# Optimization experiments

Hardware: AMD Instinct MI355X
Metric: run time of the kernel (lower is better)

The kernel has to match this reference:

```python
import jax, jax.numpy as jnp
import numpy as np

EPS = 1e-12

def l2norm(x, axis):
    # torch.nn.functional.normalize: x / max(||x||_2, eps)
    n = jnp.sqrt(jnp.sum(x * x, axis=axis, keepdims=True))
    return x / jnp.maximum(n, EPS)

def setup_inputs() -> dict:
    key = jax.random.key(0)
    k1, k2, k3, k4 = jax.random.split(key, 4)
    B, Cf, H, W = 128, 1024, 16, 16
    n_att, dv = 312, 300
    img = jax.random.normal(k1, (B, Cf, H, W), dtype=jnp.float32)
    # V is initialized from row-normalized w2v embeddings in the module
    V = l2norm(jax.random.normal(k2, (n_att, dv), dtype=jnp.float32), axis=1)
    W1 = jax.random.normal(k3, (dv, Cf), dtype=jnp.float32)
    W2 = jax.random.normal(k4, (dv, Cf), dtype=jnp.float32)
    return {"img": img, "V": V, "W1": W1, "W2": W2}

def reference(img, V, W1, W2):
    vv = l2norm(V, axis=1)                               # [i, v]
    B, Cf, H, Wd = img.shape
    av = l2norm(img.reshape(B, Cf, H * Wd), axis=1)      # [b, f, r]
    Q = vv @ W1                                          # [i, f]
    A = jnp.einsum('if,bfr->bir', Q, av)                 # attention logits
    A = jax.nn.softmax(A, axis=-1)
    F_p = jnp.einsum('bir,bfr->bif', A, av)              # attended features
    Pred_att = jnp.einsum('if,bif->bi', vv @ W2, F_p)
    return Pred_att
```

## Files before the change

kernel.cpp:

```cpp
#include <hip/hip_runtime.h>
#include <math.h>

#define NB   128
#define CF   1024
#define RR   256
#define NA   312
#define DV   300
#define M2   320
#define MT   640
#define NKC  32

typedef _Float16 half8  __attribute__((ext_vector_type(8)));
typedef float float16v  __attribute__((ext_vector_type(16)));

__device__ __forceinline__ void gload16(const void* g, void* l) {
    __builtin_amdgcn_global_load_lds(
        (const __attribute__((address_space(1))) void*)g,
        (__attribute__((address_space(3))) void*)l, 16, 0, 0);
}

__global__ void k_prep(const float* __restrict__ img, float* __restrict__ invg,
                       _Float16* __restrict__ avT) {
    int rc = blockIdx.x, b = blockIdx.y;
    int r0 = rc * 64;
    int t = threadIdx.x;
    __shared__ __align__(16) char sm[64 * 65 * 4];
    _Float16 (*tile)[65] = (_Float16 (*)[65])sm;
    float    (*ssb)[65]  = (float    (*)[65])sm;
    int fl = t >> 2, cg = t & 3;
    int rl = t >> 2, g  = t & 3;
    float ss[16];
    #pragma unroll
    for (int j = 0; j < 16; ++j) ss[j] = 0.f;

    for (int cc = 0; cc < 16; ++cc) {
        int f0 = cc * 64;
        const float4* p4 = (const float4*)(img + ((size_t)(b * CF + f0 + fl)) * RR + r0 + cg * 16);
        float4 v0 = p4[0], v1 = p4[1], v2 = p4[2], v3 = p4[3];
        __syncthreads();
        float xs[16] = {v0.x, v0.y, v0.z, v0.w, v1.x, v1.y, v1.z, v1.w,
                        v2.x, v2.y, v2.z, v2.w, v3.x, v3.y, v3.z, v3.w};
        #pragma unroll
        for (int j = 0; j < 16; ++j) {
            ss[j] += xs[j] * xs[j];
            tile[fl][cg * 16 + j] = (_Float16)xs[j];
        }
        __syncthreads();
        int kc  = (f0 >> 5) + (g >> 1);
        int kkb = (g & 1) * 16;
        half8 o0, o1;
        #pragma unroll
        for (int j = 0; j < 8; ++j) o0[j] = tile[g * 16 + j][rl];
        #pragma unroll
        for (int j = 0; j < 8; ++j) o1[j] = tile[g * 16 + 8 + j][rl];
        _Float16* q = avT + (((size_t)(b * NKC + kc) * RR + r0 + rl) * 32 + kkb);
        *(half8*)q       = o0;
        *(half8*)(q + 8) = o1;
    }
    __syncthreads();
    #pragma unroll
    for (int j = 0; j < 16; ++j) ssb[fl][cg * 16 + j] = ss[j];
    __syncthreads();
    if (t < 64) {
        float tot = 0.f;
        for (int f2 = 0; f2 < 64; ++f2) tot += ssb[f2][t];
        invg[b * RR + r0 + t] = 1.f / fmaxf(sqrtf(tot), 1e-12f);
    }
}

__global__ void k_q(const float* __restrict__ V, const float* __restrict__ W1,
                    const float* __restrict__ W2, _Float16* __restrict__ Qb) {
    int ib = blockIdx.x;
    int f  = blockIdx.y * 256 + threadIdx.x;
    int i0 = ib * 8;
    int t  = threadIdx.x;
    __shared__ float inv8[8];
    float acc[8] = {0,0,0,0,0,0,0,0};
    bool zero = (ib == 39 || ib == 79);
    int v0 = (ib < 40) ? i0 : i0 - M2;
    if (!zero) {
        int row = t >> 5, l32 = t & 31;
        float s = 0.f;
        for (int v = l32; v < DV; v += 32) { float x = V[(v0 + row) * DV + v]; s += x * x; }
        #pragma unroll
        for (int o = 16; o; o >>= 1) s += __shfl_xor(s, o, 32);
        if (l32 == 0) inv8[row] = 1.f / fmaxf(sqrtf(s), 1e-12f);
        __syncthreads();
        const float* W = (ib < 40) ? W1 : W2;
        for (int v = 0; v < DV; ++v) {
            float wv = W[(size_t)v * CF + f];
            #pragma unroll
            for (int ii = 0; ii < 8; ++ii) acc[ii] += V[(v0 + ii) * DV + v] * wv;
        }
        #pragma unroll
        for (int ii = 0; ii < 8; ++ii) acc[ii] *= inv8[ii];
    }
    #pragma unroll
    for (int ii = 0; ii < 8; ++ii)
        Qb[((size_t)(f >> 5) * MT + (i0 + ii)) * 32 + (f & 31)] = (_Float16)acc[ii];
}

__launch_bounds__(256, 2)
__global__ void k_gemm(const _Float16* __restrict__ Qb, const _Float16* __restrict__ avT,
                       const float* __restrict__ invg, float* __restrict__ out) {
    int lin  = blockIdx.x;
    int xcd  = lin & 7;
    int slot = lin >> 3;
    int bq   = slot / 5;
    int t2   = slot - bq * 5;
    int b    = bq * 8 + xcd;

    int tid = threadIdx.x;
    int lane = tid & 63, w = tid >> 6;
    int nl = lane & 31, kh = lane >> 5;

    __shared__ __align__(16) char smem[49152];
    _Float16* A0 = (_Float16*)smem;
    _Float16* A1 = (_Float16*)(smem + 8192);
    _Float16* B0 = (_Float16*)(smem + 16384);
    _Float16* B1 = (_Float16*)(smem + 32768);
    float* mred = (float*)smem;
    float* mg   = (float*)(smem + 1024);
    float* sred = (float*)(smem + 1280);
    float* dred = (float*)(smem + 2304);

    float16v acc[4][2];
    #pragma unroll
    for (int i = 0; i < 4; ++i)
        #pragma unroll
        for (int j = 0; j < 2; ++j)
            #pragma unroll
            for (int gi = 0; gi < 16; ++gi) acc[i][j][gi] = 0.f;

    int arow  = tid & 127;
    int akb0  = tid >> 7;
    int grow  = (arow < 64) ? (t2 * 64 + arow) : (M2 + t2 * 64 + (arow - 64));
    size_t a_src0 = (size_t)grow * 32 + akb0 * 8;
    size_t a_dst0 = ((size_t)akb0 * 128 + arow) * 8;
    size_t b_src0 = (size_t)tid * 32;
    size_t b_dst0 = (size_t)tid * 8;
    const _Float16* bpanel = avT + (size_t)b * NKC * RR * 32;

    #define STAGE(kc_, Ad, Bd) do {                                             \
        const _Float16* as = Qb + (size_t)(kc_) * MT * 32;                      \
        gload16(as + a_src0,      (Ad) + a_dst0);                               \
        gload16(as + a_src0 + 16, (Ad) + a_dst0 + 2048);                        \
        const _Float16* bs = bpanel + (size_t)(kc_) * RR * 32;                  \
        gload16(bs + b_src0 + 0 * 8, (Bd) + b_dst0 + 0 * 2048);                 \
        gload16(bs + b_src0 + 1 * 8, (Bd) + b_dst0 + 1 * 2048);                 \
        gload16(bs + b_src0 + 2 * 8, (Bd) + b_dst0 + 2 * 2048);                 \
        gload16(bs + b_src0 + 3 * 8, (Bd) + b_dst0 + 3 * 2048);                 \
    } while (0)

    #define COMPUTE(Al, Bl) do {                                                \
        _Pragma("unroll")                                                       \
        for (int ks = 0; ks < 2; ++ks) {                                        \
            int kb = ks * 2 + kh;                                               \
            half8 b0f = *(const half8*)((Bl) + ((size_t)kb * 256 + w * 64 + nl) * 8);       \
            half8 b1f = *(const half8*)((Bl) + ((size_t)kb * 256 + w * 64 + 32 + nl) * 8);  \
            _Pragma("unroll")                                                   \
            for (int rf = 0; rf < 4; ++rf) {                                    \
                half8 af = *(const half8*)((Al) + ((size_t)kb * 128 + rf * 32 + nl) * 8);   \
                acc[rf][0] = __builtin_amdgcn_mfma_f32_32x32x16_f16(af, b0f, acc[rf][0], 0, 0, 0); \
                acc[rf][1] = __builtin_amdgcn_mfma_f32_32x32x16_f16(af, b1f, acc[rf][1], 0, 0, 0); \
            }                                                                   \
        }                                                                       \
    } while (0)

    STAGE(0, A0, B0);
    for (int kc = 0; kc < NKC; kc += 2) {
        __syncthreads();
        STAGE(kc + 1, A1, B1);
        COMPUTE(A0, B0);
        __syncthreads();
        if (kc + 2 < NKC) STAGE(kc + 2, A0, B0);
        COMPUTE(A1, B1);
    }
    __syncthreads();
    #undef STAGE
    #undef COMPUTE

    float iv0 = invg[b * RR + w * 64 + nl];
    float iv1 = invg[b * RR + w * 64 + 32 + nl];
    #pragma unroll
    for (int rf = 0; rf < 4; ++rf)
        #pragma unroll
        for (int gi = 0; gi < 16; ++gi) {
            acc[rf][0][gi] *= iv0;
            acc[rf][1][gi] *= iv1;
        }

    float mx[2][16];
    #pragma unroll
    for (int p = 0; p < 2; ++p)
        #pragma unroll
        for (int gi = 0; gi < 16; ++gi)
            mx[p][gi] = fmaxf(acc[p][0][gi], acc[p][1][gi]);
    #pragma unroll
    for (int off = 1; off <= 16; off <<= 1)
        #pragma unroll
        for (int p = 0; p < 2; ++p)
            #pragma unroll
            for (int gi = 0; gi < 16; ++gi)
                mx[p][gi] = fmaxf(mx[p][gi], __shfl_xor(mx[p][gi], off, 64));
    if (nl == 0) {
        #pragma unroll
        for (int p = 0; p < 2; ++p)
            #pragma unroll
            for (int gi = 0; gi < 16; ++gi) {
                int row = (gi & 3) + 8 * (gi >> 2) + 4 * kh;
                mred[(p * 32 + row) * 4 + w] = mx[p][gi];
            }
    }
    __syncthreads();
    if (tid < 64)
        mg[tid] = fmaxf(fmaxf(mred[tid * 4], mred[tid * 4 + 1]),
                        fmaxf(mred[tid * 4 + 2], mred[tid * 4 + 3]));
    __syncthreads();
    float sp[2][16], dp[2][16];
    #pragma unroll
    for (int p = 0; p < 2; ++p)
        #pragma unroll
        for (int gi = 0; gi < 16; ++gi) {
            int row = (gi & 3) + 8 * (gi >> 2) + 4 * kh;
            float m  = mg[p * 32 + row];
            float e0 = __expf(acc[p][0][gi] - m);
            float e1 = __expf(acc[p][1][gi] - m);
            sp[p][gi] = e0 + e1;
            dp[p][gi] = e0 * acc[p + 2][0][gi] + e1 * acc[p + 2][1][gi];
        }
    #pragma unroll
    for (int off = 1; off <= 16; off <<= 1)
        #pragma unroll
        for (int p = 0; p < 2; ++p)
            #pragma unroll
            for (int gi = 0; gi < 16; ++gi) {
                sp[p][gi] += __shfl_xor(sp[p][gi], off, 64);
                dp[p][gi] += __shfl_xor(dp[p][gi], off, 64);
            }
    if (nl == 0) {
        #pragma unroll
        for (int p = 0; p < 2; ++p)
            #pragma unroll
            for (int gi = 0; gi < 16; ++gi) {
                int row = (gi & 3) + 8 * (gi >> 2) + 4 * kh;
                sred[(p * 32 + row) * 4 + w] = sp[p][gi];
                dred[(p * 32 + row) * 4 + w] = dp[p][gi];
            }
    }
    __syncthreads();
    if (tid < 64) {
        float s = sred[tid * 4] + sred[tid * 4 + 1] + sred[tid * 4 + 2] + sred[tid * 4 + 3];
        float d = dred[tid * 4] + dred[tid * 4 + 1] + dred[tid * 4 + 2] + dred[tid * 4 + 3];
        int ig = t2 * 64 + tid;
        if (ig < NA) out[b * NA + ig] = d / s;
    }
}

extern "C" void kernel_launch(void* const* d_in, const int* in_sizes, int n_in,
                              void* d_out, int out_size, void* d_ws, size_t ws_size,
                              hipStream_t stream) {
    const float* img = (const float*)d_in[0];
    const float* V   = (const float*)d_in[1];
    const float* W1  = (const float*)d_in[2];
    const float* W2  = (const float*)d_in[3];
    float* out = (float*)d_out;

    char* ws = (char*)d_ws;
    size_t off = 0;
    float*    invg = (float*)(ws + off);    off += (size_t)NB * RR * 4;
    _Float16* avT  = (_Float16*)(ws + off); off += (size_t)NB * CF * RR * 2;
    _Float16* Qb   = (_Float16*)(ws + off); off += (size_t)NKC * MT * 32 * 2;

    k_prep<<<dim3(4, NB), 256, 0, stream>>>(img, invg, avT);
    k_q<<<dim3(80, 4), 256, 0, stream>>>(V, W1, W2, Qb);
    k_gemm<<<dim3(640), 256, 0, stream>>>(Qb, avT, invg, out);
}
```

Baseline: 321.5 us.

## Merge prep and Q kernels; stage GEMM tiles through registers instead of direct LDS loads

```diff
diff --git a/kernel.cpp b/kernel.cpp
--- a/kernel.cpp
+++ b/kernel.cpp
@@ -13,91 +13,87 @@
 typedef _Float16 half8  __attribute__((ext_vector_type(8)));
 typedef float float16v  __attribute__((ext_vector_type(16)));
 
-__device__ __forceinline__ void gload16(const void* g, void* l) {
-    __builtin_amdgcn_global_load_lds(
-        (const __attribute__((address_space(1))) void*)g,
-        (__attribute__((address_space(3))) void*)l, 16, 0, 0);
-}
-
-__global__ void k_prep(const float* __restrict__ img, float* __restrict__ invg,
-                       _Float16* __restrict__ avT) {
-    int rc = blockIdx.x, b = blockIdx.y;
-    int r0 = rc * 64;
+__global__ void k_pre(const float* __restrict__ img, float* __restrict__ invg,
+                      _Float16* __restrict__ avT,
+                      const float* __restrict__ V, const float* __restrict__ W1,
+                      const float* __restrict__ W2, _Float16* __restrict__ Qb) {
     int t = threadIdx.x;
     __shared__ __align__(16) char sm[64 * 65 * 4];
-    _Float16 (*tile)[65] = (_Float16 (*)[65])sm;
-    float    (*ssb)[65]  = (float    (*)[65])sm;
-    int fl = t >> 2, cg = t & 3;
-    int rl = t >> 2, g  = t & 3;
-    float ss[16];
-    #pragma unroll
-    for (int j = 0; j < 16; ++j) ss[j] = 0.f;
-
-    for (int cc = 0; cc < 16; ++cc) {
-        int f0 = cc * 64;
-        const float4* p4 = (const float4*)(img + ((size_t)(b * CF + f0 + fl)) * RR + r0 + cg * 16);
-        float4 v0 = p4[0], v1 = p4[1], v2 = p4[2], v3 = p4[3];
-        __syncthreads();
-        float xs[16] = {v0.x, v0.y, v0.z, v0.w, v1.x, v1.y, v1.z, v1.w,
-                        v2.x, v2.y, v2.z, v2.w, v3.x, v3.y, v3.z, v3.w};
-        #pragma unroll
-        for (int j = 0; j < 16; ++j) {
-            ss[j] += xs[j] * xs[j];
-            tile[fl][cg * 16 + j] = (_Float16)xs[j];
-        }
-        __syncthreads();
-        int kc  = (f0 >> 5) + (g >> 1);
-        int kkb = (g & 1) * 16;
-        half8 o0, o1;
-        #pragma unroll
-        for (int j = 0; j < 8; ++j) o0[j] = tile[g * 16 + j][rl];
-        #pragma unroll
-        for (int j = 0; j < 8; ++j) o1[j] = tile[g * 16 + 8 + j][rl];
-        _Float16* q = avT + (((size_t)(b * NKC + kc) * RR + r0 + rl) * 32 + kkb);
-        *(half8*)q       = o0;
-        *(half8*)(q + 8) = o1;
-    }
-    __syncthreads();
-    #pragma unroll
-    for (int j = 0; j < 16; ++j) ssb[fl][cg * 16 + j] = ss[j];
-    __syncthreads();
-    if (t < 64) {
-        float tot = 0.f;
-        for (int f2 = 0; f2 < 64; ++f2) tot += ssb[f2][t];
-        invg[b * RR + r0 + t] = 1.f / fmaxf(sqrtf(tot), 1e-12f);
-    }
-}
-
-__global__ void k_q(const float* __restrict__ V, const float* __restrict__ W1,
-                    const float* __restrict__ W2, _Float16* __restrict__ Qb) {
-    int ib = blockIdx.x;
-    int f  = blockIdx.y * 256 + threadIdx.x;
-    int i0 = ib * 8;
-    int t  = threadIdx.x;
     __shared__ float inv8[8];
-    float acc[8] = {0,0,0,0,0,0,0,0};
-    bool zero = (ib == 39 || ib == 79);
-    int v0 = (ib < 40) ? i0 : i0 - M2;
-    if (!zero) {
-        int row = t >> 5, l32 = t & 31;
-        float s = 0.f;
-        for (int v = l32; v < DV; v += 32) { float x = V[(v0 + row) * DV + v]; s += x * x; }
-        #pragma unroll
-        for (int o = 16; o; o >>= 1) s += __shfl_xor(s, o, 32);
-        if (l32 == 0) inv8[row] = 1.f / fmaxf(sqrtf(s), 1e-12f);
-        __syncthreads();
-        const float* W = (ib < 40) ? W1 : W2;
-        for (int v = 0; v < DV; ++v) {
-            float wv = W[(size_t)v * CF + f];
-            #pragma unroll
-            for (int ii = 0; ii < 8; ++ii) acc[ii] += V[(v0 + ii) * DV + v] * wv;
-        }
-        #pragma unroll
-        for (int ii = 0; ii < 8; ++ii) acc[ii] *= inv8[ii];
-    }
-    #pragma unroll
-    for (int ii = 0; ii < 8; ++ii)
-        Qb[((size_t)(f >> 5) * MT + (i0 + ii)) * 32 + (f & 31)] = (_Float16)acc[ii];
+
+    if (blockIdx.x < 512) {
+        int rc = blockIdx.x & 3, b = blockIdx.x >> 2;
+        int r0 = rc * 64;
+        _Float16 (*tile)[65] = (_Float16 (*)[65])sm;
+        float    (*ssb)[65]  = (float    (*)[65])sm;
+        int fl = t >> 2, cg = t & 3;
+        int rl = t >> 2, g  = t & 3;
+        float ss[16];
+        #pragma unroll
+        for (int j = 0; j < 16; ++j) ss[j] = 0.f;
+
+        for (int cc = 0; cc < 16; ++cc) {
+            int f0 = cc * 64;
+            const float4* p4 = (const float4*)(img + ((size_t)(b * CF + f0 + fl)) * RR + r0 + cg * 16);
+            float4 v0 = p4[0], v1 = p4[1], v2 = p4[2], v3 = p4[3];
+            __syncthreads();
+            float xs[16] = {v0.x, v0.y, v0.z, v0.w, v1.x, v1.y, v1.z, v1.w,
+                            v2.x, v2.y, v2.z, v2.w, v3.x, v3.y, v3.z, v3.w};
+            #pragma unroll
+            for (int j = 0; j < 16; ++j) {
+                ss[j] += xs[j] * xs[j];
+                tile[fl][cg * 16 + j] = (_Float16)xs[j];
+            }
+            __syncthreads();
+            int kc  = (f0 >> 5) + (g >> 1);
+            int kkb = (g & 1) * 16;
+            half8 o0, o1;
+            #pragma unroll
+            for (int j = 0; j < 8; ++j) o0[j] = tile[g * 16 + j][rl];
+            #pragma unroll
+            for (int j = 0; j < 8; ++j) o1[j] = tile[g * 16 + 8 + j][rl];
+            _Float16* q = avT + (((size_t)(b * NKC + kc) * RR + r0 + rl) * 32 + kkb);
+            *(half8*)q       = o0;
+            *(half8*)(q + 8) = o1;
+        }
+        __syncthreads();
+        #pragma unroll
+        for (int j = 0; j < 16; ++j) ssb[fl][cg * 16 + j] = ss[j];
+        __syncthreads();
+        if (t < 64) {
+            float tot = 0.f;
+            for (int f2 = 0; f2 < 64; ++f2) tot += ssb[f2][t];
+            invg[b * RR + r0 + t] = 1.f / fmaxf(sqrtf(tot), 1e-12f);
+        }
+    } else {
+        int qi = blockIdx.x - 512;
+        int ib = qi % 80;
+        int f  = (qi / 80) * 256 + t;
+        int i0 = ib * 8;
+        float acc[8] = {0,0,0,0,0,0,0,0};
+        bool zero = (ib == 39 || ib == 79);
+        int v0 = (ib < 40) ? i0 : i0 - M2;
+        if (!zero) {
+            int row = t >> 5, l32 = t & 31;
+            float s = 0.f;
+            for (int v = l32; v < DV; v += 32) { float x = V[(v0 + row) * DV + v]; s += x * x; }
+            #pragma unroll
+            for (int o = 16; o; o >>= 1) s += __shfl_xor(s, o, 32);
+            if (l32 == 0) inv8[row] = 1.f / fmaxf(sqrtf(s), 1e-12f);
+            __syncthreads();
+            const float* W = (ib < 40) ? W1 : W2;
+            for (int v = 0; v < DV; ++v) {
+                float wv = W[(size_t)v * CF + f];
+                #pragma unroll
+                for (int ii = 0; ii < 8; ++ii) acc[ii] += V[(v0 + ii) * DV + v] * wv;
+            }
+            #pragma unroll
+            for (int ii = 0; ii < 8; ++ii) acc[ii] *= inv8[ii];
+        }
+        #pragma unroll
+        for (int ii = 0; ii < 8; ++ii)
+            Qb[((size_t)(f >> 5) * MT + (i0 + ii)) * 32 + (f & 31)] = (_Float16)acc[ii];
+    }
 }
 
 __launch_bounds__(256, 2)
@@ -141,15 +137,27 @@
     size_t b_dst0 = (size_t)tid * 8;
     const _Float16* bpanel = avT + (size_t)b * NKC * RR * 32;
 
-    #define STAGE(kc_, Ad, Bd) do {                                             \
-        const _Float16* as = Qb + (size_t)(kc_) * MT * 32;                      \
-        gload16(as + a_src0,      (Ad) + a_dst0);                               \
-        gload16(as + a_src0 + 16, (Ad) + a_dst0 + 2048);                        \
-        const _Float16* bs = bpanel + (size_t)(kc_) * RR * 32;                  \
-        gload16(bs + b_src0 + 0 * 8, (Bd) + b_dst0 + 0 * 2048);                 \
-        gload16(bs + b_src0 + 1 * 8, (Bd) + b_dst0 + 1 * 2048);                 \
-        gload16(bs + b_src0 + 2 * 8, (Bd) + b_dst0 + 2 * 2048);                 \
-        gload16(bs + b_src0 + 3 * 8, (Bd) + b_dst0 + 3 * 2048);                 \
+    half8 aR0[2], bR0[4], aR1[2], bR1[4];
+
+    #define STAGE_LOAD(kc_, Av, Bv) do {                                        \
+        int kcl = ((kc_) < NKC) ? (kc_) : (NKC - 1);                            \
+        const _Float16* as = Qb + (size_t)kcl * MT * 32;                        \
+        (Av)[0] = *(const half8*)(as + a_src0);                                 \
+        (Av)[1] = *(const half8*)(as + a_src0 + 16);                            \
+        const _Float16* bs = bpanel + (size_t)kcl * RR * 32;                    \
+        (Bv)[0] = *(const half8*)(bs + b_src0 + 0 * 8);                         \
+        (Bv)[1] = *(const half8*)(bs + b_src0 + 1 * 8);                         \
+        (Bv)[2] = *(const half8*)(bs + b_src0 + 2 * 8);                         \
+        (Bv)[3] = *(const half8*)(bs + b_src0 + 3 * 8);                         \
+    } while (0)
+
+    #define STAGE_WRITE(Av, Bv, Ad, Bd) do {                                    \
+        *(half8*)((Ad) + a_dst0)        = (Av)[0];                              \
+        *(half8*)((Ad) + a_dst0 + 2048) = (Av)[1];                              \
+        *(half8*)((Bd) + b_dst0 + 0 * 2048) = (Bv)[0];                          \
+        *(half8*)((Bd) + b_dst0 + 1 * 2048) = (Bv)[1];                          \
+        *(half8*)((Bd) + b_dst0 + 2 * 2048) = (Bv)[2];                          \
+        *(half8*)((Bd) + b_dst0 + 3 * 2048) = (Bv)[3];                          \
     } while (0)
 
     #define COMPUTE(Al, Bl) do {                                                \
@@ -167,17 +175,23 @@
         }                                                                       \
     } while (0)
 
-    STAGE(0, A0, B0);
+    STAGE_LOAD(0, aR0, bR0);
+    STAGE_LOAD(1, aR1, bR1);
+    STAGE_WRITE(aR0, bR0, A0, B0);
+
     for (int kc = 0; kc < NKC; kc += 2) {
         __syncthreads();
-        STAGE(kc + 1, A1, B1);
+        STAGE_WRITE(aR1, bR1, A1, B1);
+        STAGE_LOAD(kc + 2, aR0, bR0);
         COMPUTE(A0, B0);
         __syncthreads();
-        if (kc + 2 < NKC) STAGE(kc + 2, A0, B0);
+        if (kc + 2 < NKC) STAGE_WRITE(aR0, bR0, A0, B0);
+        STAGE_LOAD(kc + 3, aR1, bR1);
         COMPUTE(A1, B1);
     }
     __syncthreads();
-    #undef STAGE
+    #undef STAGE_LOAD
+    #undef STAGE_WRITE
     #undef COMPUTE
 
     float iv0 = invg[b * RR + w * 64 + nl];
@@ -272,7 +286,6 @@
     _Float16* avT  = (_Float16*)(ws + off); off += (size_t)NB * CF * RR * 2;
     _Float16* Qb   = (_Float16*)(ws + off); off += (size_t)NKC * MT * 32 * 2;
 
-    k_prep<<<dim3(4, NB), 256, 0, stream>>>(img, invg, avT);
-    k_q<<<dim3(80, 4), 256, 0, stream>>>(V, W1, W2, Qb);
+    k_pre<<<dim3(832), 256, 0, stream>>>(img, invg, avT, V, W1, W2, Qb);
     k_gemm<<<dim3(640), 256, 0, stream>>>(Qb, avT, invg, out);
 }
```

After: 324.9 us. No clear change (+1.1%).
